# Kernel optimization log

Measured on AMD Instinct MI355X. Metric: run time of the kernel, lower is better.

The kernel has to match this reference:

```python
import jax, jax.numpy as jnp
import numpy as np

WH, WW, NUM_HEADS = 7, 7, 16
DIM = 512
B_WINDOWS = 4096   # batch * num_windows
NW = 64            # num_windows per image (mask groups)
N = WH * WW        # 49 tokens per window


def _relative_position_index():
    # Mirrors the torch buffer construction exactly (torch.meshgrid default is 'ij').
    coords = np.stack(np.meshgrid(np.arange(WH), np.arange(WW), indexing='ij'))  # [2,WH,WW]
    cf = coords.reshape(2, -1)                              # [2, N]
    rel = cf[:, :, None] - cf[:, None, :]                   # [2, N, N]
    rel = rel.transpose(1, 2, 0).copy()                     # [N, N, 2]
    rel[:, :, 0] += WH - 1
    rel[:, :, 1] += WW - 1
    rel[:, :, 0] *= 2 * WW - 1
    return jnp.asarray(rel.sum(-1), dtype=jnp.int32)        # [N, N]

REL_IDX = _relative_position_index()


def setup_inputs() -> dict:
    key = jax.random.key(0)
    ks = jax.random.split(key, 7)
    return {
        'x':          jax.random.normal(ks[0], (B_WINDOWS, N, DIM), jnp.float32),
        'mask':       jax.random.normal(ks[1], (NW, N, N), jnp.float32),
        'Wqkv':       jax.random.normal(ks[2], (3 * DIM, DIM), jnp.float32) * (DIM ** -0.5),
        'bqkv':       jax.random.normal(ks[3], (3 * DIM,), jnp.float32) * 0.02,
        'bias_table': jax.random.normal(ks[4], ((2 * WH - 1) * (2 * WW - 1), NUM_HEADS), jnp.float32) * 0.02,
        'Wproj':      jax.random.normal(ks[5], (DIM, DIM), jnp.float32) * (DIM ** -0.5),
        'bproj':      jax.random.normal(ks[6], (DIM,), jnp.float32) * 0.02,
    }


def reference(x, mask, Wqkv, bqkv, bias_table, Wproj, bproj):
    B, n, C = x.shape                      # [B_, 49, 512]
    hd = C // NUM_HEADS
    scale = hd ** -0.5
    qkv = (x @ Wqkv.T + bqkv).reshape(B, n, 3, NUM_HEADS, hd)
    qkv = qkv.transpose(2, 0, 3, 1, 4)     # [3, B, H, N, hd]
    q, k, v = qkv[0] * scale, qkv[1], qkv[2]
    attn = jnp.einsum('bhnd,bhmd->bhnm', q, k)          # [B, H, N, N]
    # gathered relative position bias: [1, H, N, N]
    bias = bias_table[REL_IDX].transpose(2, 0, 1)[None]
    attn = attn + bias
    nW = mask.shape[0]
    attn = attn.reshape(B // nW, nW, NUM_HEADS, n, n) + mask[None, :, None]
    attn = jax.nn.softmax(attn.reshape(B, NUM_HEADS, n, n), axis=-1)
    out = jnp.einsum('bhnm,bhmd->bhnd', attn, v)        # [B, H, N, hd]
    out = out.transpose(0, 2, 1, 3).reshape(B, n, C)
    return out @ Wproj.T + bproj
```

## Files before the change

### kernel.cpp

```cpp
#include <hip/hip_runtime.h>
#include <stdint.h>

#define NHEADS 16
#define DIM 512
#define BWIN 4096
#define NTOK 49
#define M_TOTAL (BWIN * NTOK)
#define QSCALE 0.17677669529663687f

typedef __attribute__((ext_vector_type(4)))  float f32x4;
typedef __attribute__((ext_vector_type(16))) float f32x16;
typedef __attribute__((ext_vector_type(8)))  short s16x8;
typedef __attribute__((ext_vector_type(4)))  short s16x4;

__device__ __forceinline__ f32x4 mfma16(s16x8 a, s16x8 b, f32x4 c) {
    return __builtin_amdgcn_mfma_f32_16x16x32_bf16(a, b, c, 0, 0, 0);
}
__device__ __forceinline__ f32x16 mfma32(s16x8 a, s16x8 b, f32x16 c) {
    return __builtin_amdgcn_mfma_f32_32x32x16_bf16(a, b, c, 0, 0, 0);
}

__device__ __forceinline__ short f2bf(float f) {
    unsigned u = __builtin_bit_cast(unsigned, f);
    u += 0x7FFFu + ((u >> 16) & 1u);
    return (short)(u >> 16);
}

__device__ __forceinline__ unsigned cvtpk(float a, float b) {
    unsigned r;
    asm("v_cvt_pk_bf16_f32 %0, %1, %2" : "=v"(r) : "v"(a), "v"(b));
    return r;
}

__device__ __forceinline__ void gload16(const void* g, void* l) {
    __builtin_amdgcn_global_load_lds(
        (const __attribute__((address_space(1))) void*)g,
        (__attribute__((address_space(3))) void*)l, 16, 0, 0);
}


__global__ void k_prep_x(const float* __restrict__ x, short* __restrict__ xb) {
    int i = blockIdx.x * blockDim.x + threadIdx.x;
    int stride = gridDim.x * blockDim.x;
    const int n4 = M_TOTAL * DIM / 4;
    for (; i < n4; i += stride) {
        f32x4 v = ((const f32x4*)x)[i];
        s16x4 o;
        o[0] = f2bf(v[0]); o[1] = f2bf(v[1]); o[2] = f2bf(v[2]); o[3] = f2bf(v[3]);
        ((s16x4*)xb)[i] = o;
    }
}

__global__ void k_prep_w(const float* __restrict__ src, short* __restrict__ dst,
                         int n, int scale_lim) {
    int i = blockIdx.x * blockDim.x + threadIdx.x;
    int stride = gridDim.x * blockDim.x;
    for (; i < n; i += stride) {
        float v = src[i];
        if (i < scale_lim) v *= QSCALE;
        dst[i] = f2bf(v);
    }
}

__global__ void k_prep_bm(const float* __restrict__ btab, const float* __restrict__ mask,
                          float* __restrict__ bmT) {
    int idx = blockIdx.x * blockDim.x + threadIdx.x;
    int stride = gridDim.x * blockDim.x;
    const int n = 64 * NHEADS * 49 * 64;
    for (; idx < n; idx += stride) {
        int i = idx & 63;
        int rest = idx >> 6;
        int j = rest % 49;
        int wh = rest / 49;
        int head = wh & 15;
        int w64 = wh >> 4;
        float v = 0.f;
        if (i < 49) {
            int ridx = (i / 7 - j / 7 + 6) * 13 + (i % 7 - j % 7 + 6);
            v = btab[ridx * 16 + head] + mask[(w64 * 49 + i) * 49 + j];
        }
        bmT[idx] = v;
    }
}

template <int MODE>
__global__ __launch_bounds__(512, 2) void k_gemm(
    const short* __restrict__ A, const short* __restrict__ B,
    const float* __restrict__ bias, void* __restrict__ C,
    int ntiles, int nwg) {
    __shared__ short lA[2][256 * 64];
    __shared__ short lB[2][256 * 64];
    const int K = 512;
    const size_t MP = M_TOTAL;

    int bid   = blockIdx.x;
    int chunk = nwg >> 3;
    int wg    = (bid & 7) * chunk + (bid >> 3);
    int mt = wg / ntiles;
    int nt = wg - mt * ntiles;

    int t = threadIdx.x;
    int lane = t & 63, wid = t >> 6;
    int l15 = lane & 15, g = (lane >> 4) & 3;
    int wr = wid >> 2, wc = wid & 3;

    int srow = t >> 3;
    int schunk = (t & 7) ^ (srow & 7);
    const short* aSrc = A + (size_t)(mt * 256 + srow) * K + schunk * 8;
    const short* bSrc = B + (size_t)(nt * 256 + srow) * K + schunk * 8;
    const int dstOff = t * 8;

    f32x4 acc[8][4] = {};

#define STAGE(buf, k0)                                                        \
    _Pragma("unroll")                                                         \
    for (int i = 0; i < 4; i++) {                                             \
        gload16(aSrc + (size_t)i * 64 * K + (k0), &lA[buf][i * 4096 + dstOff]); \
        gload16(bSrc + (size_t)i * 64 * K + (k0), &lB[buf][i * 4096 + dstOff]); \
    }

    STAGE(0, 0)
    for (int kt = 0; kt < 8; ++kt) {
        if (kt < 7) {
            STAGE((kt + 1) & 1, (kt + 1) * 64)
            asm volatile("s_waitcnt vmcnt(8)" ::: "memory");
        } else {
            asm volatile("s_waitcnt vmcnt(0)" ::: "memory");
        }
        __builtin_amdgcn_s_barrier();

        const short* pa = &lA[kt & 1][(wr * 128 + l15) * 64];
        const short* pb = &lB[kt & 1][(wc * 64 + l15) * 64];
        const int sw = l15 & 7;
#pragma unroll
        for (int ks = 0; ks < 2; ks++) {
            s16x8 af[8], bf[4];
#pragma unroll
            for (int mi = 0; mi < 8; mi++)
                af[mi] = *(const s16x8*)(pa + mi * 1024 + (((ks * 4 + g) ^ sw) * 8));
#pragma unroll
            for (int nj = 0; nj < 4; nj++)
                bf[nj] = *(const s16x8*)(pb + nj * 1024 + (((ks * 4 + g) ^ sw) * 8));
#pragma unroll
            for (int mi = 0; mi < 8; mi++)
#pragma unroll
                for (int nj = 0; nj < 4; nj++)
                    acc[mi][nj] = mfma16(af[mi], bf[nj], acc[mi][nj]);
        }
        __builtin_amdgcn_s_barrier();
    }
#undef STAGE

    int m0 = mt * 256 + wr * 128;
    int n0 = nt * 256 + wc * 64;

    if (MODE == 0) {
        short* region = (wid < 4) ? (&lA[0][0] + wid * 8192)
                                  : (&lB[0][0] + (wid - 4) * 8192);
#pragma unroll
        for (int nj = 0; nj < 4; nj++) {
            int n = n0 + nj * 16 + l15;
            float bv = bias[n];
            if (n < 512) bv *= QSCALE;
            int w16 = nj * 2 + (l15 >> 3);
#pragma unroll
            for (int mi = 0; mi < 8; mi++)
#pragma unroll
                for (int r = 0; r < 4; r++) {
                    int row = mi * 16 + g * 4 + r;
                    region[row * 64 + ((w16 ^ (row & 7)) * 8) + (l15 & 7)] =
                        f2bf(acc[mi][nj][r] + bv);
                }
        }
#pragma unroll
        for (int p = 0; p < 2; p++) {
            int plane = (n0 >> 5) + p;
            short* dst = (short*)C + ((size_t)plane * MP + m0) * 32;
#pragma unroll
            for (int i = 0; i < 8; i++) {
                int f = i * 64 + lane;
                int row = f >> 2, c = f & 3;
                s16x8 v = *(const s16x8*)(region + row * 64 +
                                          (((p * 4 + c) ^ (row & 7)) * 8));
                *(s16x8*)(dst + (size_t)f * 8) = v;
            }
        }
    } else {
#pragma unroll
        for (int nj = 0; nj < 4; nj++) {
            int n = n0 + nj * 16 + l15;
            float bv = bias[n];
#pragma unroll
            for (int mi = 0; mi < 8; mi++)
#pragma unroll
                for (int r = 0; r < 4; r++) {
                    int m = m0 + mi * 16 + g * 4 + r;
                    ((float*)C)[(size_t)m * 512 + n] = acc[mi][nj][r] + bv;
                }
        }
    }
}

__global__ __launch_bounds__(256, 4) void k_attn(
    const short* __restrict__ qkv, const float* __restrict__ bmT,
    short* __restrict__ ao) {
    int wid = threadIdx.x >> 6, lane = threadIdx.x & 63;
    int p = blockIdx.x * 4 + wid;
    int w = p >> 4, head = p & 15;
    int l31 = lane & 31, h = lane >> 5;
    const size_t MP = M_TOTAL;

    const short* qb = qkv + ((size_t)head * MP + w * 49) * 32;
    const short* kb = qb + (size_t)16 * MP * 32;
    const short* vb = qb + (size_t)32 * MP * 32;

    s16x8 qf[2][2], kf[2][2];
#pragma unroll
    for (int t = 0; t < 2; t++) {
        int row = t * 32 + l31;
#pragma unroll
        for (int s = 0; s < 2; s++) {
            qf[t][s] = *(const s16x8*)(qb + row * 32 + 16 * s + 8 * h);
            kf[t][s] = *(const s16x8*)(kb + row * 32 + 16 * s + 8 * h);
        }
    }

    union U8 { short s[8]; s16x8 v; };
    U8 vf[4];
#pragma unroll
    for (int jc = 0; jc < 4; jc++)
#pragma unroll
        for (int e = 0; e < 8; e++)
            vf[jc].s[e] = vb[(16 * jc + 8 * h + e) * 32 + l31];

    f32x16 st[2][2] = {};
#pragma unroll
    for (int s = 0; s < 2; s++)
#pragma unroll
        for (int jt = 0; jt < 2; jt++)
#pragma unroll
            for (int it = 0; it < 2; it++)
                st[jt][it] = mfma32(kf[jt][s], qf[it][s], st[jt][it]);

    const float* bs = bmT + ((size_t)((w & 63) * NHEADS + head)) * 3136 + l31;
#pragma unroll
    for (int jt = 0; jt < 2; jt++)
#pragma unroll
        for (int it = 0; it < 2; it++)
#pragma unroll
            for (int r = 0; r < 16; r++) {
                int j = 32 * jt + (r & 3) + 8 * (r >> 2) + 4 * h;
                if (j < 49) st[jt][it][r] += bs[j * 64 + 32 * it];
                else        st[jt][it][r] = -1e30f;
            }

    float inv[2];
#pragma unroll
    for (int it = 0; it < 2; it++) {
        float mx = -1e30f;
#pragma unroll
        for (int jt = 0; jt < 2; jt++)
#pragma unroll
            for (int r = 0; r < 16; r++) mx = fmaxf(mx, st[jt][it][r]);
        mx = fmaxf(mx, __shfl_xor(mx, 32));
        float sum = 0.f;
#pragma unroll
        for (int jt = 0; jt < 2; jt++)
#pragma unroll
            for (int r = 0; r < 16; r++) {
                float e = __expf(st[jt][it][r] - mx);
                st[jt][it][r] = e;
                sum += e;
            }
        sum += __shfl_xor(sum, 32);
        inv[it] = 1.0f / sum;
    }

    f32x16 oacc[2] = {};
#pragma unroll
    for (int jc = 0; jc < 4; jc++) {
        const int jt = jc >> 1, rb = 8 * (jc & 1);
#pragma unroll
        for (int it = 0; it < 2; it++) {
            float iv = inv[it];
            unsigned pk0  = cvtpk(st[jt][it][rb + 0] * iv, st[jt][it][rb + 1] * iv);
            unsigned pk0b = cvtpk(st[jt][it][rb + 2] * iv, st[jt][it][rb + 3] * iv);
            unsigned pk1  = cvtpk(st[jt][it][rb + 4] * iv, st[jt][it][rb + 5] * iv);
            unsigned pk1b = cvtpk(st[jt][it][rb + 6] * iv, st[jt][it][rb + 7] * iv);
            unsigned o0  = __shfl_xor(pk0, 32);
            unsigned o0b = __shfl_xor(pk0b, 32);
            unsigned o1  = __shfl_xor(pk1, 32);
            unsigned o1b = __shfl_xor(pk1b, 32);
            union { unsigned d[4]; s16x8 v; } pa;
            pa.d[0] = h ? o1  : pk0;
            pa.d[1] = h ? o1b : pk0b;
            pa.d[2] = h ? pk1 : o0;
            pa.d[3] = h ? pk1b : o0b;
            oacc[it] = mfma32(pa.v, vf[jc].v, oacc[it]);
        }
    }

    short* ob = ao + (size_t)w * 49 * 512 + head * 32 + l31;
#pragma unroll
    for (int it = 0; it < 2; it++)
#pragma unroll
        for (int r = 0; r < 16; r++) {
            int i = 32 * it + 4 * h + (r & 3) + 8 * (r >> 2);
            if (i < 49) ob[(size_t)i * 512] = f2bf(oacc[it][r]);
        }
}


extern "C" void kernel_launch(void* const* d_in, const int* in_sizes, int n_in,
                              void* d_out, int out_size, void* d_ws, size_t ws_size,
                              hipStream_t stream) {
    const float* x     = (const float*)d_in[0];
    const float* mask  = (const float*)d_in[1];
    const float* Wqkv  = (const float*)d_in[2];
    const float* bqkv  = (const float*)d_in[3];
    const float* btab  = (const float*)d_in[4];
    const float* Wproj = (const float*)d_in[5];
    const float* bproj = (const float*)d_in[6];
    float* out = (float*)d_out;

    char* ws = (char*)d_ws;
    size_t off = 0;
    short* xb     = (short*)(ws + off); off += (size_t)M_TOTAL * 512 * 2;
    short* qkvb   = (short*)(ws + off); off += (size_t)48 * M_TOTAL * 32 * 2 + 65536;
    short* Wqkvb  = (short*)(ws + off); off += (size_t)1536 * 512 * 2;
    short* Wprojb = (short*)(ws + off); off += (size_t)512 * 512 * 2;
    float* bmT    = (float*)(ws + off); off += (size_t)64 * NHEADS * 49 * 64 * 4;
    short* ao = xb;

    k_prep_x<<<2048, 256, 0, stream>>>(x, xb);
    k_prep_w<<<1536, 256, 0, stream>>>(Wqkv, Wqkvb, 1536 * 512, 512 * 512);
    k_prep_w<<<512, 256, 0, stream>>>(Wproj, Wprojb, 512 * 512, 0);
    k_prep_bm<<<2048, 256, 0, stream>>>(btab, mask, bmT);

    k_gemm<0><<<4704, 512, 0, stream>>>(xb, Wqkvb, bqkv, qkvb, 6, 4704);
    k_attn<<<16384, 256, 0, stream>>>(qkvb, bmT, ao);
    k_gemm<1><<<1568, 512, 0, stream>>>(ao, Wprojb, bproj, out, 2, 1568);
}
```

Before: 1.178 ms.

## Split GEMM k-step into four quadrant phases interleaving staging with MFMA

Restructures the GEMM main loop so each k-tile runs as four quadrant phases (A-half × B-half). Each phase loads LDS fragments, issues a partial global-to-LDS stage for the next tile, then runs MFMAs at raised wave priority. The goal is to overlap global loads and LDS reads with matrix math and to cut register pressure from holding full fragment sets. The cost is more barriers per k-step and a remapped B-row layout, which the epilogue has to mirror through the changed column indexing.

```diff
diff --git a/kernel.cpp b/kernel.cpp
--- a/kernel.cpp
+++ b/kernel.cpp
@@ -104,52 +104,101 @@
     int l15 = lane & 15, g = (lane >> 4) & 3;
     int wr = wid >> 2, wc = wid & 3;
 
-    int srow = t >> 3;
-    int schunk = (t & 7) ^ (srow & 7);
-    const short* aSrc = A + (size_t)(mt * 256 + srow) * K + schunk * 8;
-    const short* bSrc = B + (size_t)(nt * 256 + srow) * K + schunk * 8;
-    const int dstOff = t * 8;
+    const short* aT = A + (size_t)mt * 256 * K;
+    const short* bT = B + (size_t)nt * 256 * K;
 
     f32x4 acc[8][4] = {};
-
-#define STAGE(buf, k0)                                                        \
-    _Pragma("unroll")                                                         \
-    for (int i = 0; i < 4; i++) {                                             \
-        gload16(aSrc + (size_t)i * 64 * K + (k0), &lA[buf][i * 4096 + dstOff]); \
-        gload16(bSrc + (size_t)i * 64 * K + (k0), &lB[buf][i * 4096 + dstOff]); \
-    }
-
-    STAGE(0, 0)
+    s16x8 af[4][2], bf0[2][2], bf1[2][2];
+
+#define STAGE_A(buf, H, kt) do {                                               \
+    _Pragma("unroll") for (int j = 0; j < 2; j++) {                            \
+        int r_ = j * 128 + (H) * 64 + (t >> 3);                                \
+        int sc_ = (t & 7) ^ (r_ & 7);                                          \
+        gload16(aT + (size_t)r_ * K + (kt) * 64 + sc_ * 8,                     \
+                &lA[buf][r_ * 64 + (t & 7) * 8]);                              \
+    } } while (0)
+
+#define STAGE_B(buf, H, kt) do {                                               \
+    _Pragma("unroll") for (int j = 0; j < 2; j++) {                            \
+        int u_ = j * 64 + (t >> 3);                                            \
+        int r_ = ((u_ >> 5) << 6) | ((H) << 5) | (u_ & 31);                    \
+        int sc_ = (t & 7) ^ (r_ & 7);                                          \
+        gload16(bT + (size_t)r_ * K + (kt) * 64 + sc_ * 8,                     \
+                &lB[buf][r_ * 64 + (t & 7) * 8]);                              \
+    } } while (0)
+
+#define LDA(MH, cur) do {                                                      \
+    const short* pa_ = &lA[cur][(wr * 128 + (MH) * 64 + l15) * 64];            \
+    _Pragma("unroll") for (int mi = 0; mi < 4; mi++)                           \
+    _Pragma("unroll") for (int ks = 0; ks < 2; ks++)                           \
+        af[mi][ks] = *(const s16x8*)(pa_ + mi * 1024 +                         \
+                                     (((ks * 4 + g) ^ (l15 & 7)) * 8));        \
+    } while (0)
+
+#define LDB(BF, NH, cur) do {                                                  \
+    const short* pb_ = &lB[cur][(wc * 64 + (NH) * 32 + l15) * 64];             \
+    _Pragma("unroll") for (int nj = 0; nj < 2; nj++)                           \
+    _Pragma("unroll") for (int ks = 0; ks < 2; ks++)                           \
+        BF[nj][ks] = *(const s16x8*)(pb_ + nj * 1024 +                         \
+                                     (((ks * 4 + g) ^ (l15 & 7)) * 8));        \
+    } while (0)
+
+#define MMQ(BF, MH, NH) do {                                                   \
+    __builtin_amdgcn_s_setprio(1);                                             \
+    _Pragma("unroll") for (int ks = 0; ks < 2; ks++)                           \
+    _Pragma("unroll") for (int mi = 0; mi < 4; mi++)                           \
+    _Pragma("unroll") for (int nj = 0; nj < 2; nj++)                           \
+        acc[(MH) * 4 + mi][(NH) * 2 + nj] =                                    \
+            mfma16(af[mi][ks], BF[nj][ks], acc[(MH) * 4 + mi][(NH) * 2 + nj]); \
+    __builtin_amdgcn_s_setprio(0);                                             \
+} while (0)
+
+#define BAR() __builtin_amdgcn_s_barrier()
+#define LGW() do { asm volatile("s_waitcnt lgkmcnt(0)" ::: "memory");          \
+                   __builtin_amdgcn_sched_barrier(0); } while (0)
+#define VMW(st) do {                                                           \
+    if (st) asm volatile("s_waitcnt vmcnt(4)" ::: "memory");                   \
+    else    asm volatile("s_waitcnt vmcnt(0)" ::: "memory"); } while (0)
+
+    STAGE_A(0, 0, 0);
+    STAGE_B(0, 0, 0);
+    STAGE_B(0, 1, 0);
+    STAGE_A(0, 1, 0);
+    asm volatile("s_waitcnt vmcnt(4)" ::: "memory");
+    BAR();
+
     for (int kt = 0; kt < 8; ++kt) {
-        if (kt < 7) {
-            STAGE((kt + 1) & 1, (kt + 1) * 64)
-            asm volatile("s_waitcnt vmcnt(8)" ::: "memory");
-        } else {
-            asm volatile("s_waitcnt vmcnt(0)" ::: "memory");
-        }
-        __builtin_amdgcn_s_barrier();
-
-        const short* pa = &lA[kt & 1][(wr * 128 + l15) * 64];
-        const short* pb = &lB[kt & 1][(wc * 64 + l15) * 64];
-        const int sw = l15 & 7;
-#pragma unroll
-        for (int ks = 0; ks < 2; ks++) {
-            s16x8 af[8], bf[4];
-#pragma unroll
-            for (int mi = 0; mi < 8; mi++)
-                af[mi] = *(const s16x8*)(pa + mi * 1024 + (((ks * 4 + g) ^ sw) * 8));
-#pragma unroll
-            for (int nj = 0; nj < 4; nj++)
-                bf[nj] = *(const s16x8*)(pb + nj * 1024 + (((ks * 4 + g) ^ sw) * 8));
-#pragma unroll
-            for (int mi = 0; mi < 8; mi++)
-#pragma unroll
-                for (int nj = 0; nj < 4; nj++)
-                    acc[mi][nj] = mfma16(af[mi], bf[nj], acc[mi][nj]);
-        }
-        __builtin_amdgcn_s_barrier();
-    }
-#undef STAGE
+        const int cur = kt & 1, nxt = cur ^ 1;
+        const bool st = kt < 7;
+        LDA(0, cur); LDB(bf0, 0, cur);
+        if (st) STAGE_A(nxt, 0, kt + 1);
+        VMW(st); BAR(); LGW();
+        MMQ(bf0, 0, 0);
+        BAR();
+        LDB(bf1, 1, cur);
+        if (st) STAGE_B(nxt, 0, kt + 1);
+        VMW(st); BAR(); LGW();
+        MMQ(bf1, 0, 1);
+        BAR();
+        LDA(1, cur);
+        if (st) STAGE_B(nxt, 1, kt + 1);
+        VMW(st); BAR(); LGW();
+        MMQ(bf1, 1, 1);
+        BAR();
+        if (st) STAGE_A(nxt, 1, kt + 1);
+        VMW(st); BAR(); LGW();
+        MMQ(bf0, 1, 0);
+        BAR();
+    }
+
+#undef STAGE_A
+#undef STAGE_B
+#undef LDA
+#undef LDB
+#undef MMQ
+#undef BAR
+#undef LGW
+#undef VMW
 
     int m0 = mt * 256 + wr * 128;
     int n0 = nt * 256 + wc * 64;
@@ -158,18 +207,19 @@
         short* region = (wid < 4) ? (&lA[0][0] + wid * 8192)
                                   : (&lB[0][0] + (wid - 4) * 8192);
 #pragma unroll
-        for (int nj = 0; nj < 4; nj++) {
-            int n = n0 + nj * 16 + l15;
+        for (int a = 0; a < 4; a++) {
+            int co = (a >> 1) * 32 + (a & 1) * 16;
+            int n = n0 + co + l15;
             float bv = bias[n];
             if (n < 512) bv *= QSCALE;
-            int w16 = nj * 2 + (l15 >> 3);
+            int w16 = (co >> 3) + (l15 >> 3);
 #pragma unroll
             for (int mi = 0; mi < 8; mi++)
 #pragma unroll
                 for (int r = 0; r < 4; r++) {
                     int row = mi * 16 + g * 4 + r;
                     region[row * 64 + ((w16 ^ (row & 7)) * 8) + (l15 & 7)] =
-                        f2bf(acc[mi][nj][r] + bv);
+                        f2bf(acc[mi][a][r] + bv);
                 }
         }
 #pragma unroll
@@ -187,15 +237,16 @@
         }
     } else {
 #pragma unroll
-        for (int nj = 0; nj < 4; nj++) {
-            int n = n0 + nj * 16 + l15;
+        for (int a = 0; a < 4; a++) {
+            int co = (a >> 1) * 32 + (a & 1) * 16;
+            int n = n0 + co + l15;
             float bv = bias[n];
 #pragma unroll
             for (int mi = 0; mi < 8; mi++)
 #pragma unroll
                 for (int r = 0; r < 4; r++) {
                     int m = m0 + mi * 16 + g * 4 + r;
-                    ((float*)C)[(size_t)m * 512 + n] = acc[mi][nj][r] + bv;
+                    ((float*)C)[(size_t)m * 512 + n] = acc[mi][a][r] + bv;
                 }
         }
     }
```

After: 1.164 ms. About the same (-1.2%).

## Fuse fp32-to-bf16 conversion of x into QKV GEMM with 32x32 MFMA pipeline

Applied to the files above, without the earlier changes.

Drops the separate x-conversion kernel. The QKV GEMM now loads fp32 x from global memory, converts it to bf16 in registers and writes it to LDS, which removes one full write and read of a 200MB activation tensor. The GEMM main loop is also restructured to use 32x32x16 MFMAs in four quarter-steps, with loads interleaved between them, priority hints and finer barriers. Risks are more register pressure and heavier fp32 global traffic in the QKV GEMM, where x is loaded directly in fp32 instead of as pre-converted bf16.

```diff
diff --git a/kernel.cpp b/kernel.cpp
--- a/kernel.cpp
+++ b/kernel.cpp
@@ -13,9 +13,6 @@
 typedef __attribute__((ext_vector_type(8)))  short s16x8;
 typedef __attribute__((ext_vector_type(4)))  short s16x4;
 
-__device__ __forceinline__ f32x4 mfma16(s16x8 a, s16x8 b, f32x4 c) {
-    return __builtin_amdgcn_mfma_f32_16x16x32_bf16(a, b, c, 0, 0, 0);
-}
 __device__ __forceinline__ f32x16 mfma32(s16x8 a, s16x8 b, f32x16 c) {
     return __builtin_amdgcn_mfma_f32_32x32x16_bf16(a, b, c, 0, 0, 0);
 }
@@ -38,18 +35,6 @@
         (__attribute__((address_space(3))) void*)l, 16, 0, 0);
 }
 
-
-__global__ void k_prep_x(const float* __restrict__ x, short* __restrict__ xb) {
-    int i = blockIdx.x * blockDim.x + threadIdx.x;
-    int stride = gridDim.x * blockDim.x;
-    const int n4 = M_TOTAL * DIM / 4;
-    for (; i < n4; i += stride) {
-        f32x4 v = ((const f32x4*)x)[i];
-        s16x4 o;
-        o[0] = f2bf(v[0]); o[1] = f2bf(v[1]); o[2] = f2bf(v[2]); o[3] = f2bf(v[3]);
-        ((s16x4*)xb)[i] = o;
-    }
-}
 
 __global__ void k_prep_w(const float* __restrict__ src, short* __restrict__ dst,
                          int n, int scale_lim) {
@@ -85,7 +70,8 @@
 
 template <int MODE>
 __global__ __launch_bounds__(512, 2) void k_gemm(
-    const short* __restrict__ A, const short* __restrict__ B,
+    const float* __restrict__ Af, const short* __restrict__ Ab,
+    const short* __restrict__ B,
     const float* __restrict__ bias, void* __restrict__ C,
     int ntiles, int nwg) {
     __shared__ short lA[2][256 * 64];
@@ -101,75 +87,178 @@
 
     int t = threadIdx.x;
     int lane = t & 63, wid = t >> 6;
-    int l15 = lane & 15, g = (lane >> 4) & 3;
+    int l31 = lane & 31, h = lane >> 5;
     int wr = wid >> 2, wc = wid & 3;
-
-    int srow = t >> 3;
-    int schunk = (t & 7) ^ (srow & 7);
-    const short* aSrc = A + (size_t)(mt * 256 + srow) * K + schunk * 8;
-    const short* bSrc = B + (size_t)(nt * 256 + srow) * K + schunk * 8;
-    const int dstOff = t * 8;
-
-    f32x4 acc[8][4] = {};
-
-#define STAGE(buf, k0)                                                        \
-    _Pragma("unroll")                                                         \
-    for (int i = 0; i < 4; i++) {                                             \
-        gload16(aSrc + (size_t)i * 64 * K + (k0), &lA[buf][i * 4096 + dstOff]); \
-        gload16(bSrc + (size_t)i * 64 * K + (k0), &lB[buf][i * 4096 + dstOff]); \
-    }
-
-    STAGE(0, 0)
+    int wslot = (t & 7) ^ ((t >> 3) & 7);
+
+    const short* aTb = Ab + (size_t)mt * 256 * K;
+    const float* aTf = Af + (size_t)mt * 256 * K;
+    const short* bT  = B  + (size_t)nt * 256 * K;
+
+    f32x16 acc[4][2] = {};
+    s16x8 afr[2][4], bfr[4];
+    f32x4 cqa0, cqa1, cqb0, cqb1, lqa0, lqa1, lqb0, lqb1;
+
+#define STAGE_A(buf, H, kt) do {                                               \
+    _Pragma("unroll") for (int j = 0; j < 2; j++) {                            \
+        int r_ = j * 128 + (H) * 64 + (t >> 3);                                \
+        int sc_ = (t & 7) ^ (r_ & 7);                                          \
+        gload16(aTb + (size_t)r_ * K + (kt) * 64 + sc_ * 8,                    \
+                &lA[buf][r_ * 64 + (t & 7) * 8]);                              \
+    } } while (0)
+
+#define STAGE_B(buf, H, kt) do {                                               \
+    _Pragma("unroll") for (int j = 0; j < 2; j++) {                            \
+        int u_ = j * 64 + (t >> 3);                                            \
+        int r_ = ((u_ >> 5) << 6) | ((H) << 5) | (u_ & 31);                    \
+        int sc_ = (t & 7) ^ (r_ & 7);                                          \
+        gload16(bT + (size_t)r_ * K + (kt) * 64 + sc_ * 8,                     \
+                &lB[buf][r_ * 64 + (t & 7) * 8]);                              \
+    } } while (0)
+
+#define LOADA(rb, kt2, r0, r1) do {                                            \
+    const float* ps_ = aTf + ((size_t)((rb) + (t >> 3))) * K + (kt2) * 64 +    \
+                       (t & 7) * 8;                                            \
+    r0 = *(const f32x4*)ps_; r1 = *(const f32x4*)(ps_ + 4); } while (0)
+
+#define WRA(buf, rb, r0, r1) do {                                              \
+    union { unsigned d[4]; s16x8 v; } u_;                                      \
+    u_.d[0] = cvtpk(r0[0], r0[1]); u_.d[1] = cvtpk(r0[2], r0[3]);              \
+    u_.d[2] = cvtpk(r1[0], r1[1]); u_.d[3] = cvtpk(r1[2], r1[3]);              \
+    *(s16x8*)(&lA[buf][((rb) + (t >> 3)) * 64 + wslot * 8]) = u_.v; } while (0)
+
+#define LDA32(AH, cur) do {                                                    \
+    const short* pa_ = &lA[cur][(wr * 128 + (AH) * 64 + l31) * 64];            \
+    _Pragma("unroll") for (int a2 = 0; a2 < 2; a2++)                           \
+    _Pragma("unroll") for (int ks = 0; ks < 4; ks++)                           \
+        afr[a2][ks] = *(const s16x8*)(pa_ + a2 * 2048 +                        \
+                                      (((ks * 2 + h) ^ (l31 & 7)) * 8));       \
+    } while (0)
+
+#define LDB32(BH, cur) do {                                                    \
+    const short* pb_ = &lB[cur][(wc * 64 + (BH) * 32 + l31) * 64];             \
+    _Pragma("unroll") for (int ks = 0; ks < 4; ks++)                           \
+        bfr[ks] = *(const s16x8*)(pb_ + (((ks * 2 + h) ^ (l31 & 7)) * 8));     \
+    } while (0)
+
+#define MMQ32(AH, BH) do {                                                     \
+    __builtin_amdgcn_s_setprio(1);                                             \
+    _Pragma("unroll") for (int ks = 0; ks < 4; ks++)                           \
+    _Pragma("unroll") for (int a2 = 0; a2 < 2; a2++)                           \
+        acc[(AH) * 2 + a2][BH] =                                               \
+            mfma32(afr[a2][ks], bfr[ks], acc[(AH) * 2 + a2][BH]);              \
+    __builtin_amdgcn_s_setprio(0);                                             \
+} while (0)
+
+#define PWAIT(s) do {                                                          \
+    if (s) { if (MODE == 0)                                                    \
+                 asm volatile("s_waitcnt vmcnt(6) lgkmcnt(0)" ::: "memory");   \
+             else                                                              \
+                 asm volatile("s_waitcnt vmcnt(4) lgkmcnt(0)" ::: "memory"); } \
+    else asm volatile("s_waitcnt vmcnt(0) lgkmcnt(0)" ::: "memory");           \
+} while (0)
+
+#define BARP() do { __builtin_amdgcn_s_barrier();                              \
+                    __builtin_amdgcn_sched_barrier(0); } while (0)
+
+    if constexpr (MODE == 0) {
+        STAGE_B(0, 0, 0); STAGE_B(0, 1, 0);
+#pragma unroll
+        for (int c = 0; c < 4; c++) {
+            int rb = (c & 1) * 128 + (c >> 1) * 64;
+            f32x4 ta, tb;
+            LOADA(rb, 0, ta, tb);
+            WRA(0, rb, ta, tb);
+        }
+        LOADA(0,   1, cqa0, cqa1);
+        LOADA(128, 1, cqb0, cqb1);
+        asm volatile("s_waitcnt vmcnt(4) lgkmcnt(0)" ::: "memory");
+    } else {
+        STAGE_A(0, 0, 0); STAGE_B(0, 0, 0);
+        STAGE_B(0, 1, 0); STAGE_A(0, 1, 0);
+        asm volatile("s_waitcnt vmcnt(0) lgkmcnt(0)" ::: "memory");
+    }
+    BARP();
+
     for (int kt = 0; kt < 8; ++kt) {
-        if (kt < 7) {
-            STAGE((kt + 1) & 1, (kt + 1) * 64)
-            asm volatile("s_waitcnt vmcnt(8)" ::: "memory");
+        const int cur = kt & 1, nxt = cur ^ 1;
+        const bool s7 = kt < 7, s6 = kt < 6;
+        LDA32(0, cur); LDB32(0, cur);
+        if constexpr (MODE == 0) {
+            if (s7) {
+                STAGE_B(nxt, 0, kt + 1);
+                LOADA(64, kt + 1, lqa0, lqa1);
+                WRA(nxt, 0, cqa0, cqa1);
+            }
         } else {
-            asm volatile("s_waitcnt vmcnt(0)" ::: "memory");
-        }
-        __builtin_amdgcn_s_barrier();
-
-        const short* pa = &lA[kt & 1][(wr * 128 + l15) * 64];
-        const short* pb = &lB[kt & 1][(wc * 64 + l15) * 64];
-        const int sw = l15 & 7;
-#pragma unroll
-        for (int ks = 0; ks < 2; ks++) {
-            s16x8 af[8], bf[4];
-#pragma unroll
-            for (int mi = 0; mi < 8; mi++)
-                af[mi] = *(const s16x8*)(pa + mi * 1024 + (((ks * 4 + g) ^ sw) * 8));
-#pragma unroll
-            for (int nj = 0; nj < 4; nj++)
-                bf[nj] = *(const s16x8*)(pb + nj * 1024 + (((ks * 4 + g) ^ sw) * 8));
-#pragma unroll
-            for (int mi = 0; mi < 8; mi++)
-#pragma unroll
-                for (int nj = 0; nj < 4; nj++)
-                    acc[mi][nj] = mfma16(af[mi], bf[nj], acc[mi][nj]);
-        }
-        __builtin_amdgcn_s_barrier();
-    }
-#undef STAGE
+            if (s7) STAGE_A(nxt, 0, kt + 1);
+        }
+        PWAIT(s7);
+        MMQ32(0, 0);
+        BARP();
+        LDB32(1, cur);
+        if constexpr (MODE == 0) {
+            if (s7) {
+                STAGE_B(nxt, 1, kt + 1);
+                LOADA(192, kt + 1, lqb0, lqb1);
+                WRA(nxt, 128, cqb0, cqb1);
+            }
+        } else {
+            if (s7) STAGE_B(nxt, 0, kt + 1);
+        }
+        PWAIT(s7);
+        MMQ32(0, 1);
+        BARP();
+        LDA32(1, cur);
+        if constexpr (MODE == 0) {
+            if (s6) LOADA(0, kt + 2, cqa0, cqa1);
+            if (s7) WRA(nxt, 64, lqa0, lqa1);
+        } else {
+            if (s7) STAGE_B(nxt, 1, kt + 1);
+        }
+        PWAIT(s7);
+        MMQ32(1, 1);
+        BARP();
+        LDB32(0, cur);
+        if constexpr (MODE == 0) {
+            if (s6) LOADA(128, kt + 2, cqb0, cqb1);
+            if (s7) WRA(nxt, 192, lqb0, lqb1);
+        } else {
+            if (s7) STAGE_A(nxt, 1, kt + 1);
+        }
+        PWAIT(s7);
+        MMQ32(1, 0);
+        BARP();
+    }
+
+#undef STAGE_A
+#undef STAGE_B
+#undef LOADA
+#undef WRA
+#undef LDA32
+#undef LDB32
+#undef MMQ32
+#undef PWAIT
+#undef BARP
 
     int m0 = mt * 256 + wr * 128;
     int n0 = nt * 256 + wc * 64;
-
-    if (MODE == 0) {
+    if constexpr (MODE == 0) {
         short* region = (wid < 4) ? (&lA[0][0] + wid * 8192)
                                   : (&lB[0][0] + (wid - 4) * 8192);
 #pragma unroll
-        for (int nj = 0; nj < 4; nj++) {
-            int n = n0 + nj * 16 + l15;
+        for (int bt = 0; bt < 2; bt++) {
+            int n = n0 + bt * 32 + l31;
             float bv = bias[n];
             if (n < 512) bv *= QSCALE;
-            int w16 = nj * 2 + (l15 >> 3);
-#pragma unroll
-            for (int mi = 0; mi < 8; mi++)
-#pragma unroll
-                for (int r = 0; r < 4; r++) {
-                    int row = mi * 16 + g * 4 + r;
-                    region[row * 64 + ((w16 ^ (row & 7)) * 8) + (l15 & 7)] =
-                        f2bf(acc[mi][nj][r] + bv);
+            int cchunk = bt * 4 + (l31 >> 3);
+#pragma unroll
+            for (int at = 0; at < 4; at++)
+#pragma unroll
+                for (int r = 0; r < 16; r++) {
+                    int row = at * 32 + 4 * h + (r & 3) + 8 * (r >> 2);
+                    region[row * 64 + ((cchunk ^ (row & 7)) * 8) + (l31 & 7)] =
+                        f2bf(acc[at][bt][r] + bv);
                 }
         }
 #pragma unroll
@@ -187,15 +276,15 @@
         }
     } else {
 #pragma unroll
-        for (int nj = 0; nj < 4; nj++) {
-            int n = n0 + nj * 16 + l15;
+        for (int bt = 0; bt < 2; bt++) {
+            int n = n0 + bt * 32 + l31;
             float bv = bias[n];
 #pragma unroll
-            for (int mi = 0; mi < 8; mi++)
-#pragma unroll
-                for (int r = 0; r < 4; r++) {
-                    int m = m0 + mi * 16 + g * 4 + r;
-                    ((float*)C)[(size_t)m * 512 + n] = acc[mi][nj][r] + bv;
+            for (int at = 0; at < 4; at++)
+#pragma unroll
+                for (int r = 0; r < 16; r++) {
+                    int m = m0 + at * 32 + 4 * h + (r & 3) + 8 * (r >> 2);
+                    ((float*)C)[(size_t)m * 512 + n] = acc[at][bt][r] + bv;
                 }
         }
     }
@@ -325,19 +414,17 @@
 
     char* ws = (char*)d_ws;
     size_t off = 0;
-    short* xb     = (short*)(ws + off); off += (size_t)M_TOTAL * 512 * 2;
+    short* ao     = (short*)(ws + off); off += (size_t)M_TOTAL * 512 * 2;
     short* qkvb   = (short*)(ws + off); off += (size_t)48 * M_TOTAL * 32 * 2 + 65536;
     short* Wqkvb  = (short*)(ws + off); off += (size_t)1536 * 512 * 2;
     short* Wprojb = (short*)(ws + off); off += (size_t)512 * 512 * 2;
     float* bmT    = (float*)(ws + off); off += (size_t)64 * NHEADS * 49 * 64 * 4;
-    short* ao = xb;
-
-    k_prep_x<<<2048, 256, 0, stream>>>(x, xb);
+
     k_prep_w<<<1536, 256, 0, stream>>>(Wqkv, Wqkvb, 1536 * 512, 512 * 512);
     k_prep_w<<<512, 256, 0, stream>>>(Wproj, Wprojb, 512 * 512, 0);
     k_prep_bm<<<2048, 256, 0, stream>>>(btab, mask, bmT);
 
-    k_gemm<0><<<4704, 512, 0, stream>>>(xb, Wqkvb, bqkv, qkvb, 6, 4704);
+    k_gemm<0><<<4704, 512, 0, stream>>>(x, nullptr, Wqkvb, bqkv, qkvb, 6, 4704);
     k_attn<<<16384, 256, 0, stream>>>(qkvb, bmT, ao);
-    k_gemm<1><<<1568, 512, 0, stream>>>(ao, Wprojb, bproj, out, 2, 1568);
-}
+    k_gemm<1><<<1568, 512, 0, stream>>>(nullptr, ao, Wprojb, bproj, out, 2, 1568);
+}
```

Measured after the change: 1.153 ms. -2.1%, faster.
